# Optimization experiments

Hardware: AMD Instinct MI355X
Metric: run time of the kernel (lower is better)

## Reference

```python
import jax, jax.numpy as jnp
import numpy as np

T, INPUT, POP_EXC, POP_INH = 128, 2048, 2048, 512
DT = 1e-3
TAU_SYN_INV, TAU_MEM_INV = 200.0, 100.0
V_LEAK, V_TH, V_RESET = 0.0, 1.0, 0.0
RHO_RESET = 5.0            # refractory counter reset (in steps)
ALPHA = 100.0              # SuperSpike surrogate slope (used in bwd variant)
A_PRE = A_POST = 1.0
TAU_PRE_INV = TAU_POST_INV = 50.0
ETA_PLUS = ETA_MINUS = 1e-3
W_MIN, W_MAX = 0.0, 1.0


def heaviside(x):
    return (x > 0).astype(x.dtype)


def lif_refrac_step(inp, v, i, rho):
    # norse LIF feed-forward step
    v_dec = v + DT * TAU_MEM_INV * ((V_LEAK - v) + i)
    i_dec = i * (1.0 - DT * TAU_SYN_INV)
    z = heaviside(v_dec - V_TH)
    v_new = (1.0 - z) * v_dec + z * V_RESET
    i_new = i_dec + inp
    # refractory update
    refrac = heaviside(rho)                      # neurons still refractory
    v_new = (1.0 - refrac) * v_new + refrac * V_RESET
    z = (1.0 - refrac) * z
    rho_new = (1.0 - z) * jax.nn.relu(rho - refrac) + z * RHO_RESET
    return z, v_new, i_new, rho_new


def stdp_step(z_pre, z_post, w, t_pre, t_post):
    # additive STDP (norse stdp_step_linear, mu=0) with trace low-pass filters
    t_pre = t_pre + DT * TAU_PRE_INV * (-t_pre + A_PRE * z_pre)
    t_post = t_post + DT * TAU_POST_INV * (-t_post + A_POST * z_post)
    dw = ETA_PLUS * jnp.outer(z_post, t_pre) - ETA_MINUS * jnp.outer(t_post, z_pre)
    w = jnp.clip(w + dw, W_MIN, W_MAX)           # (post, pre)
    return w, t_pre, t_post


def setup_inputs() -> dict:
    key = jax.random.key(0)
    k1, k2, k3 = jax.random.split(key, 3)
    exc_currents = 2.0 * jax.random.uniform(k1, (T, INPUT), dtype=jnp.float32)
    w_exc = 0.05 * jax.random.uniform(k2, (POP_EXC, INPUT), dtype=jnp.float32)
    w_inh = 0.05 * jax.random.uniform(k3, (POP_INH, POP_EXC), dtype=jnp.float32)
    return {"exc_currents": exc_currents, "w_exc": w_exc, "w_inh": w_inh}


def reference(exc_currents, w_exc, w_inh):
    zf = jnp.zeros
    carry0 = (
        w_exc, zf(POP_EXC), zf(POP_EXC), zf(POP_EXC),   # w, v, i, rho (exc)
        zf(INPUT), zf(POP_EXC),                         # t_pre, t_post (exc)
        w_inh, zf(POP_INH), zf(POP_INH), zf(POP_INH),   # w, v, i, rho (inh)
        zf(POP_EXC), zf(POP_INH),                       # t_pre, t_post (inh)
    )

    def step(c, x):
        (we, ve, ie, re, tpe, tqe, wi, vi, ii, ri, tpi, tqi) = c
        # excitatory STDP layer: matvec input current, LIF-refrac, STDP update
        z_e, ve, ie, re = lif_refrac_step(x @ we.T, ve, ie, re)
        we, tpe, tqe = stdp_step(x, z_e, we, tpe, tqe)
        # inhibitory STDP layer driven by excitatory spikes
        z_i, vi, ii, ri = lif_refrac_step(z_e @ wi.T, vi, ii, ri)
        wi, tpi, tqi = stdp_step(z_e, z_i, wi, tpi, tqi)
        return (we, ve, ie, re, tpe, tqe, wi, vi, ii, ri, tpi, tqi), z_e

    _, spikes = jax.lax.scan(step, carry0, exc_currents)
    return spikes  # [T, POP_EXC]
```

## Files before the change

### kernel.cpp

```cpp
#include <hip/hip_runtime.h>


constexpr int T_STEPS = 128;
constexpr int N_IN    = 2048;
constexpr int N_EXC   = 2048;
constexpr int HALF    = N_IN / 2;

__global__ __launch_bounds__(256)
void tp_precompute_kernel(const float* __restrict__ x, float* __restrict__ tp_ws) {
    const int j = blockIdx.x * blockDim.x + threadIdx.x;
    float tp = 0.f;
    #pragma unroll 4
    for (int t = 0; t < T_STEPS; ++t) {
        tp = fmaf(0.05f, x[t * N_IN + j] - tp, tp);
        tp_ws[t * N_IN + j] = tp;
    }
}

template <int CTRL, int RM>
__device__ __forceinline__ float dpp_add(float x) {
    int t = __builtin_amdgcn_update_dpp(0, __builtin_bit_cast(int, x),
                                        CTRL, RM, 0xF, true);
    return x + __builtin_bit_cast(float, t);
}

__device__ __forceinline__ float wave_sum64_to_lane63(float x) {
    x = dpp_add<0x111, 0xF>(x);
    x = dpp_add<0x112, 0xF>(x);
    x = dpp_add<0x114, 0xF>(x);
    x = dpp_add<0x118, 0xF>(x);
    x = dpp_add<0x142, 0xA>(x);
    x = dpp_add<0x143, 0xC>(x);
    return x;
}

__global__ __launch_bounds__(256, 4)
void snn_exc_kernel(const float* __restrict__ x,
                    const float* __restrict__ w0,
                    const float* __restrict__ tp_ws,
                    float* __restrict__ out)
{
    __shared__ float part[2][2][2];

    const int tid  = threadIdx.x;
    const int lane = tid & 63;
    const int wid  = tid >> 6;
    const int ni   = wid >> 1;
    const int half = wid & 1;
    const int row  = blockIdx.x * 2 + ni;

    float w[16];
    {
        const float4* wrow = reinterpret_cast<const float4*>(
            w0 + (size_t)row * N_IN + half * HALF);
        #pragma unroll
        for (int m = 0; m < 4; ++m) {
            float4 t4 = wrow[m * 64 + lane];
            w[4*m+0] = t4.x; w[4*m+1] = t4.y; w[4*m+2] = t4.z; w[4*m+3] = t4.w;
        }
    }

    const float4* xbase = reinterpret_cast<const float4*>(x) + half * (HALF / 4) + lane;
    const float4* tpb   = reinterpret_cast<const float4*>(tp_ws) + half * (HALF / 4) + lane;

    float4 xa[4], xb[4];
    #pragma unroll
    for (int m = 0; m < 4; ++m) xa[m] = xbase[m * 64];

    if (tid < 8) reinterpret_cast<float*>(part)[tid] = 0.f;
    __syncthreads();

    float v = 0.f, syn = 0.f, rho = 0.f, tpost = 0.f;

    auto step = [&](int t, const float4 (&xc)[4], float4 (&xn)[4]) {
        const int tn = (t + 1 < T_STEPS) ? (t + 1) : (T_STEPS - 1);
        const float4* xv = xbase + (size_t)tn * (N_IN / 4);
        #pragma unroll
        for (int m = 0; m < 4; ++m) xn[m] = xv[m * 64];

        const float p0 = part[(t + 1) & 1][ni][0];
        const float p1 = part[(t + 1) & 1][ni][1];
        syn = fmaf(0.8f, syn, p0 + p1);

        const float v_dec = fmaf(0.1f, syn - v, v);
        const bool refrac = (rho > 0.f);
        const bool spike  = (v_dec > 1.0f) && !refrac;
        v   = (spike || refrac) ? 0.f : v_dec;
        rho = spike ? 5.0f : fmaxf(rho - (refrac ? 1.f : 0.f), 0.f);
        const float zf = spike ? 1.f : 0.f;
        tpost = fmaf(0.05f, zf - tpost, tpost);
        const float c2 = 1e-3f * tpost;
        if (half == 0 && lane == 0) out[t * N_EXC + row] = zf;

        float4 tq[4];
        if (spike) {
            const float4* tq4 = tpb + (size_t)t * (N_IN / 4);
            #pragma unroll
            for (int m = 0; m < 4; ++m) tq[m] = tq4[m * 64];
        }

        float a0 = 0.f, a1 = 0.f, a2 = 0.f, a3 = 0.f;
        #pragma unroll
        for (int m = 0; m < 4; ++m) {
            a0 = fmaf(xc[m].x, w[4*m+0], a0);
            a1 = fmaf(xc[m].y, w[4*m+1], a1);
            a2 = fmaf(xc[m].z, w[4*m+2], a2);
            a3 = fmaf(xc[m].w, w[4*m+3], a3);
        }

        if (spike) {
            #pragma unroll
            for (int m = 0; m < 4; ++m) {
                w[4*m+0] = fmaxf(fmaf(1e-3f, tq[m].x, fmaf(-c2, xc[m].x, w[4*m+0])), 0.f);
                w[4*m+1] = fmaxf(fmaf(1e-3f, tq[m].y, fmaf(-c2, xc[m].y, w[4*m+1])), 0.f);
                w[4*m+2] = fmaxf(fmaf(1e-3f, tq[m].z, fmaf(-c2, xc[m].z, w[4*m+2])), 0.f);
                w[4*m+3] = fmaxf(fmaf(1e-3f, tq[m].w, fmaf(-c2, xc[m].w, w[4*m+3])), 0.f);
            }
        } else {
            #pragma unroll
            for (int m = 0; m < 4; ++m) {
                w[4*m+0] = fmaxf(fmaf(-c2, xc[m].x, w[4*m+0]), 0.f);
                w[4*m+1] = fmaxf(fmaf(-c2, xc[m].y, w[4*m+1]), 0.f);
                w[4*m+2] = fmaxf(fmaf(-c2, xc[m].z, w[4*m+2]), 0.f);
                w[4*m+3] = fmaxf(fmaf(-c2, xc[m].w, w[4*m+3]), 0.f);
            }
        }

        const float s = wave_sum64_to_lane63((a0 + a1) + (a2 + a3));
        if (lane == 63) part[t & 1][ni][half] = s;
        __syncthreads();
    };

    for (int t = 0; t < T_STEPS; t += 2) {
        step(t,     xa, xb);
        step(t + 1, xb, xa);
    }
}

extern "C" void kernel_launch(void* const* d_in, const int* in_sizes, int n_in,
                              void* d_out, int out_size, void* d_ws, size_t ws_size,
                              hipStream_t stream) {
    const float* x  = (const float*)d_in[0];
    const float* w0 = (const float*)d_in[1];
    float* out = (float*)d_out;

    float* tp_ws = (float*)d_ws;
    tp_precompute_kernel<<<N_IN / 256, 256, 0, stream>>>(x, tp_ws);

    dim3 grid(N_EXC / 2);
    dim3 block(256);
    snn_exc_kernel<<<grid, block, 0, stream>>>(x, w0, tp_ws, out);
}
```

Baseline: 102.5 us.

## Process two excitatory neurons per wave to share input loads

Each wave now keeps weights for two output neurons and reuses the same x and pre-trace loads for both matvec partials and STDP updates. The grid is halved, and the partial-sum write moves ahead of the weight update so the reduction no longer waits on the STDP arithmetic. Spike branches use readfirstlane to keep control flow uniform across the wave, and clamping uses fmed3. The cost is double the register footprint (launch bounds lowered to 2 blocks per SIMD) and fewer blocks in flight, which lowers parallelism for the latency-bound time loop.

```diff
diff --git a/kernel.cpp b/kernel.cpp
--- a/kernel.cpp
+++ b/kernel.cpp
@@ -4,13 +4,13 @@
 constexpr int T_STEPS = 128;
 constexpr int N_IN    = 2048;
 constexpr int N_EXC   = 2048;
-constexpr int HALF    = N_IN / 2;
+constexpr int HALF    = 1024;
 
 __global__ __launch_bounds__(256)
 void tp_precompute_kernel(const float* __restrict__ x, float* __restrict__ tp_ws) {
     const int j = blockIdx.x * blockDim.x + threadIdx.x;
     float tp = 0.f;
-    #pragma unroll 4
+    #pragma unroll 16
     for (int t = 0; t < T_STEPS; ++t) {
         tp = fmaf(0.05f, x[t * N_IN + j] - tp, tp);
         tp_ws[t * N_IN + j] = tp;
@@ -34,100 +34,150 @@
     return x;
 }
 
-__global__ __launch_bounds__(256, 4)
+__device__ __forceinline__ float clamp01(float x) {
+    return __builtin_amdgcn_fmed3f(x, 0.f, 1.f);
+}
+
+__global__ __launch_bounds__(256, 2)
 void snn_exc_kernel(const float* __restrict__ x,
                     const float* __restrict__ w0,
                     const float* __restrict__ tp_ws,
                     float* __restrict__ out)
 {
-    __shared__ float part[2][2][2];
+    __shared__ float part[2][2][2][2];
 
     const int tid  = threadIdx.x;
     const int lane = tid & 63;
     const int wid  = tid >> 6;
-    const int ni   = wid >> 1;
-    const int half = wid & 1;
-    const int row  = blockIdx.x * 2 + ni;
-
-    float w[16];
+    const int p    = wid >> 1;
+    const int h    = wid & 1;
+    const int rA   = blockIdx.x * 4 + 2 * p;
+
+    float wA[16], wB[16];
     {
-        const float4* wrow = reinterpret_cast<const float4*>(
-            w0 + (size_t)row * N_IN + half * HALF);
+        const float4* ra = reinterpret_cast<const float4*>(w0 + (size_t)rA * N_IN + h * HALF);
+        const float4* rb = reinterpret_cast<const float4*>(w0 + (size_t)(rA + 1) * N_IN + h * HALF);
         #pragma unroll
         for (int m = 0; m < 4; ++m) {
-            float4 t4 = wrow[m * 64 + lane];
-            w[4*m+0] = t4.x; w[4*m+1] = t4.y; w[4*m+2] = t4.z; w[4*m+3] = t4.w;
+            float4 a = ra[m * 64 + lane];
+            float4 b = rb[m * 64 + lane];
+            wA[4*m+0] = a.x; wA[4*m+1] = a.y; wA[4*m+2] = a.z; wA[4*m+3] = a.w;
+            wB[4*m+0] = b.x; wB[4*m+1] = b.y; wB[4*m+2] = b.z; wB[4*m+3] = b.w;
         }
     }
 
-    const float4* xbase = reinterpret_cast<const float4*>(x) + half * (HALF / 4) + lane;
-    const float4* tpb   = reinterpret_cast<const float4*>(tp_ws) + half * (HALF / 4) + lane;
+    const float4* xsl = reinterpret_cast<const float4*>(x + h * HALF) + lane;
+    const float4* tps = reinterpret_cast<const float4*>(tp_ws + h * HALF) + lane;
+
+    if (tid < 16) reinterpret_cast<float*>(part)[tid] = 0.f;
 
     float4 xa[4], xb[4];
     #pragma unroll
-    for (int m = 0; m < 4; ++m) xa[m] = xbase[m * 64];
-
-    if (tid < 8) reinterpret_cast<float*>(part)[tid] = 0.f;
+    for (int m = 0; m < 4; ++m) xa[m] = xsl[m * 64];
     __syncthreads();
 
-    float v = 0.f, syn = 0.f, rho = 0.f, tpost = 0.f;
+    float vA = 0.f, synA = 0.f, rhoA = 0.f, tpostA = 0.f;
+    float vB = 0.f, synB = 0.f, rhoB = 0.f, tpostB = 0.f;
 
     auto step = [&](int t, const float4 (&xc)[4], float4 (&xn)[4]) {
-        const int tn = (t + 1 < T_STEPS) ? (t + 1) : (T_STEPS - 1);
-        const float4* xv = xbase + (size_t)tn * (N_IN / 4);
+        int tn = t + 1; if (tn > T_STEPS - 1) tn = T_STEPS - 1;
+        const float4* xp = xsl + (size_t)tn * (N_IN / 4);
         #pragma unroll
-        for (int m = 0; m < 4; ++m) xn[m] = xv[m * 64];
-
-        const float p0 = part[(t + 1) & 1][ni][0];
-        const float p1 = part[(t + 1) & 1][ni][1];
-        syn = fmaf(0.8f, syn, p0 + p1);
-
-        const float v_dec = fmaf(0.1f, syn - v, v);
-        const bool refrac = (rho > 0.f);
-        const bool spike  = (v_dec > 1.0f) && !refrac;
-        v   = (spike || refrac) ? 0.f : v_dec;
-        rho = spike ? 5.0f : fmaxf(rho - (refrac ? 1.f : 0.f), 0.f);
-        const float zf = spike ? 1.f : 0.f;
-        tpost = fmaf(0.05f, zf - tpost, tpost);
-        const float c2 = 1e-3f * tpost;
-        if (half == 0 && lane == 0) out[t * N_EXC + row] = zf;
+        for (int m = 0; m < 4; ++m) xn[m] = xp[m * 64];
+
+        const float4 pp = *reinterpret_cast<const float4*>(&part[t & 1][p][0][0]);
+        synA = fmaf(0.8f, synA, pp.x + pp.z);
+        synB = fmaf(0.8f, synB, pp.y + pp.w);
+
+        const float vdA = fmaf(0.1f, synA - vA, vA);
+        const bool  rfA = (rhoA > 0.f);
+        const bool  kA  = (vdA > 1.0f) && !rfA;
+        vA     = (kA || rfA) ? 0.f : vdA;
+        rhoA   = kA ? 5.0f : fmaxf(rhoA - 1.0f, 0.f);
+        const float zA = kA ? 1.f : 0.f;
+        tpostA = fmaf(0.05f, zA - tpostA, tpostA);
+        const float c2A = 1e-3f * tpostA;
+
+        const float vdB = fmaf(0.1f, synB - vB, vB);
+        const bool  rfB = (rhoB > 0.f);
+        const bool  kB  = (vdB > 1.0f) && !rfB;
+        vB     = (kB || rfB) ? 0.f : vdB;
+        rhoB   = kB ? 5.0f : fmaxf(rhoB - 1.0f, 0.f);
+        const float zB = kB ? 1.f : 0.f;
+        tpostB = fmaf(0.05f, zB - tpostB, tpostB);
+        const float c2B = 1e-3f * tpostB;
+
+        if (h == 0 && lane == 0) {
+            float2 zz; zz.x = zA; zz.y = zB;
+            *reinterpret_cast<float2*>(out + (size_t)t * N_EXC + rA) = zz;
+        }
+
+        const int sA = __builtin_amdgcn_readfirstlane((int)kA);
+        const int sB = __builtin_amdgcn_readfirstlane((int)kB);
 
         float4 tq[4];
-        if (spike) {
-            const float4* tq4 = tpb + (size_t)t * (N_IN / 4);
-            #pragma unroll
-            for (int m = 0; m < 4; ++m) tq[m] = tq4[m * 64];
+        if (sA | sB) {
+            const float4* tp4 = tps + (size_t)t * (N_IN / 4);
+            #pragma unroll
+            for (int m = 0; m < 4; ++m) tq[m] = tp4[m * 64];
         }
 
         float a0 = 0.f, a1 = 0.f, a2 = 0.f, a3 = 0.f;
+        float b0 = 0.f, b1 = 0.f, b2 = 0.f, b3 = 0.f;
         #pragma unroll
         for (int m = 0; m < 4; ++m) {
-            a0 = fmaf(xc[m].x, w[4*m+0], a0);
-            a1 = fmaf(xc[m].y, w[4*m+1], a1);
-            a2 = fmaf(xc[m].z, w[4*m+2], a2);
-            a3 = fmaf(xc[m].w, w[4*m+3], a3);
-        }
-
-        if (spike) {
-            #pragma unroll
-            for (int m = 0; m < 4; ++m) {
-                w[4*m+0] = fmaxf(fmaf(1e-3f, tq[m].x, fmaf(-c2, xc[m].x, w[4*m+0])), 0.f);
-                w[4*m+1] = fmaxf(fmaf(1e-3f, tq[m].y, fmaf(-c2, xc[m].y, w[4*m+1])), 0.f);
-                w[4*m+2] = fmaxf(fmaf(1e-3f, tq[m].z, fmaf(-c2, xc[m].z, w[4*m+2])), 0.f);
-                w[4*m+3] = fmaxf(fmaf(1e-3f, tq[m].w, fmaf(-c2, xc[m].w, w[4*m+3])), 0.f);
+            a0 = fmaf(xc[m].x, wA[4*m+0], a0);
+            b0 = fmaf(xc[m].x, wB[4*m+0], b0);
+            a1 = fmaf(xc[m].y, wA[4*m+1], a1);
+            b1 = fmaf(xc[m].y, wB[4*m+1], b1);
+            a2 = fmaf(xc[m].z, wA[4*m+2], a2);
+            b2 = fmaf(xc[m].z, wB[4*m+2], b2);
+            a3 = fmaf(xc[m].w, wA[4*m+3], a3);
+            b3 = fmaf(xc[m].w, wB[4*m+3], b3);
+        }
+
+        const float sAr = wave_sum64_to_lane63((a0 + a1) + (a2 + a3));
+        const float sBr = wave_sum64_to_lane63((b0 + b1) + (b2 + b3));
+        if (lane == 63) {
+            float2 pw; pw.x = sAr; pw.y = sBr;
+            *reinterpret_cast<float2*>(&part[(t + 1) & 1][p][h][0]) = pw;
+        }
+
+        if (sA) {
+            #pragma unroll
+            for (int m = 0; m < 4; ++m) {
+                wA[4*m+0] = clamp01(fmaf(1e-3f, tq[m].x, fmaf(-c2A, xc[m].x, wA[4*m+0])));
+                wA[4*m+1] = clamp01(fmaf(1e-3f, tq[m].y, fmaf(-c2A, xc[m].y, wA[4*m+1])));
+                wA[4*m+2] = clamp01(fmaf(1e-3f, tq[m].z, fmaf(-c2A, xc[m].z, wA[4*m+2])));
+                wA[4*m+3] = clamp01(fmaf(1e-3f, tq[m].w, fmaf(-c2A, xc[m].w, wA[4*m+3])));
             }
         } else {
             #pragma unroll
             for (int m = 0; m < 4; ++m) {
-                w[4*m+0] = fmaxf(fmaf(-c2, xc[m].x, w[4*m+0]), 0.f);
-                w[4*m+1] = fmaxf(fmaf(-c2, xc[m].y, w[4*m+1]), 0.f);
-                w[4*m+2] = fmaxf(fmaf(-c2, xc[m].z, w[4*m+2]), 0.f);
-                w[4*m+3] = fmaxf(fmaf(-c2, xc[m].w, w[4*m+3]), 0.f);
-            }
-        }
-
-        const float s = wave_sum64_to_lane63((a0 + a1) + (a2 + a3));
-        if (lane == 63) part[t & 1][ni][half] = s;
+                wA[4*m+0] = clamp01(fmaf(-c2A, xc[m].x, wA[4*m+0]));
+                wA[4*m+1] = clamp01(fmaf(-c2A, xc[m].y, wA[4*m+1]));
+                wA[4*m+2] = clamp01(fmaf(-c2A, xc[m].z, wA[4*m+2]));
+                wA[4*m+3] = clamp01(fmaf(-c2A, xc[m].w, wA[4*m+3]));
+            }
+        }
+        if (sB) {
+            #pragma unroll
+            for (int m = 0; m < 4; ++m) {
+                wB[4*m+0] = clamp01(fmaf(1e-3f, tq[m].x, fmaf(-c2B, xc[m].x, wB[4*m+0])));
+                wB[4*m+1] = clamp01(fmaf(1e-3f, tq[m].y, fmaf(-c2B, xc[m].y, wB[4*m+1])));
+                wB[4*m+2] = clamp01(fmaf(1e-3f, tq[m].z, fmaf(-c2B, xc[m].z, wB[4*m+2])));
+                wB[4*m+3] = clamp01(fmaf(1e-3f, tq[m].w, fmaf(-c2B, xc[m].w, wB[4*m+3])));
+            }
+        } else {
+            #pragma unroll
+            for (int m = 0; m < 4; ++m) {
+                wB[4*m+0] = clamp01(fmaf(-c2B, xc[m].x, wB[4*m+0]));
+                wB[4*m+1] = clamp01(fmaf(-c2B, xc[m].y, wB[4*m+1]));
+                wB[4*m+2] = clamp01(fmaf(-c2B, xc[m].z, wB[4*m+2]));
+                wB[4*m+3] = clamp01(fmaf(-c2B, xc[m].w, wB[4*m+3]));
+            }
+        }
+
         __syncthreads();
     };
 
@@ -147,7 +197,7 @@
     float* tp_ws = (float*)d_ws;
     tp_precompute_kernel<<<N_IN / 256, 256, 0, stream>>>(x, tp_ws);
 
-    dim3 grid(N_EXC / 2);
+    dim3 grid(N_EXC / 4);
     dim3 block(256);
     snn_exc_kernel<<<grid, block, 0, stream>>>(x, w0, tp_ws, out);
 }
```

After: 90.74 us. 1.13x faster.
